# Kernel tuning notes

Measured on AMD Instinct MI355X. Metric: run time of the kernel, lower is better.

Reference implementation:

```python
import jax, jax.numpy as jnp
import numpy as np

HEADS = 8
DIM_HEAD = 128
LN_EPS = 1e-5


def setup_inputs() -> dict:
    key = jax.random.key(0)
    ks = jax.random.split(key, 4)
    N, M, C, V, T = 64, 2, 64, 15, 256
    dim = C * V              # 960
    inner = HEADS * DIM_HEAD # 1024
    return {
        "x": jax.random.normal(ks[0], (N, M, C, V, T), dtype=jnp.float32),
        "ln_g": jnp.ones((dim,), jnp.float32),
        "ln_b": jnp.zeros((dim,), jnp.float32),
        "w_qkv": jax.random.normal(ks[1], (dim, 3 * inner), dtype=jnp.float32) * (dim ** -0.5),
        "w_out": jax.random.normal(ks[2], (inner, dim), dtype=jnp.float32) * (inner ** -0.5),
        "b_out": jnp.zeros((dim,), jnp.float32),
        "w_lin": jax.random.normal(ks[3], (T, T), dtype=jnp.float32) * (T ** -0.5),
        "b_lin": jnp.zeros((T,), jnp.float32),
    }


def reference(x, ln_g, ln_b, w_qkv, w_out, b_out, w_lin, b_lin):
    N, M, C, V, T = x.shape
    dim = C * V
    # [N, M, C, V, T] -> [N*M, T, C*V]
    xs = jnp.transpose(x, (0, 1, 4, 2, 3)).reshape(N * M, T, dim)

    # PreNorm (LayerNorm over last dim)
    mu = jnp.mean(xs, axis=-1, keepdims=True)
    var = jnp.mean(jnp.square(xs - mu), axis=-1, keepdims=True)
    xn = (xs - mu) * jax.lax.rsqrt(var + LN_EPS) * ln_g + ln_b

    # Attention
    qkv = xn @ w_qkv  # [NM, T, 3*inner]
    q, k, v = jnp.split(qkv, 3, axis=-1)
    def to_heads(t):
        return jnp.transpose(t.reshape(N * M, T, HEADS, DIM_HEAD), (0, 2, 1, 3))
    q, k, v = to_heads(q), to_heads(k), to_heads(v)  # [NM, H, T, D]
    scale = DIM_HEAD ** -0.5
    dots = jnp.einsum('nhid,nhjd->nhij', q, k) * scale
    attn = jax.nn.softmax(dots, axis=-1)
    out = jnp.einsum('nhij,nhjd->nhid', attn, v)
    out = jnp.transpose(out, (0, 2, 1, 3)).reshape(N * M, T, HEADS * DIM_HEAD)
    out = out @ w_out + b_out

    # Residual
    xs = out + xs

    # back to [N, M, C, V, T], then Linear over T + tanh
    x2 = jnp.transpose(xs.reshape(N, M, T, C, V), (0, 1, 3, 4, 2))
    y = jnp.tanh(x2 @ w_lin.T + b_lin)
    return y
```

## Files before the change

kernel.cpp:

```cpp
#include <hip/hip_runtime.h>

typedef unsigned short ushort;
using short8 = __attribute__((ext_vector_type(8))) short;
using f32x4  = __attribute__((ext_vector_type(4))) float;
using i32x4  = __attribute__((ext_vector_type(4))) int;
using us4    = __attribute__((ext_vector_type(4))) ushort;

static __device__ __forceinline__ float bf2f(ushort u) {
  union { unsigned int i; float f; } x; x.i = ((unsigned int)u) << 16; return x.f;
}
static __device__ __forceinline__ ushort f2bf(float f) {
  union { float f; unsigned int i; } x; x.f = f;
  unsigned int u = x.i;
  unsigned int r = u + 0x7fffu + ((u >> 16) & 1u);
  return (ushort)(r >> 16);
}

#define GLOAD16(gp, lp)                                                   \
  __builtin_amdgcn_global_load_lds(                                      \
      (const __attribute__((address_space(1))) void*)(gp),               \
      (__attribute__((address_space(3))) void*)(lp), 16, 0, 0)

__global__ __launch_bounds__(256) void wtrans_kernel(const float* __restrict__ in,
                                                     ushort* __restrict__ out,
                                                     int R, int C) {
  __shared__ float sl[32][33];
  int tx = threadIdx.x & 31, ty = threadIdx.x >> 5;
  int c0 = blockIdx.x * 32, r0 = blockIdx.y * 32;
#pragma unroll
  for (int s = 0; s < 4; s++) {
    int r = r0 + ty + s * 8;
    int c = c0 + tx;
    sl[ty + s * 8][tx] = (c < C) ? in[(size_t)r * C + c] : 0.f;
  }
  __syncthreads();
#pragma unroll
  for (int s = 0; s < 4; s++) {
    int c = c0 + ty + s * 8;
    int r = r0 + tx;
    out[(size_t)c * R + r] = f2bf(sl[tx][ty + s * 8]);
  }
}

__global__ void wsplit_kernel(const float* __restrict__ in, ushort* __restrict__ hi,
                              ushort* __restrict__ lo, int n) {
  int i = blockIdx.x * 256 + threadIdx.x;
  if (i < n) {
    float v = in[i];
    ushort h = f2bf(v);
    hi[i] = h;
    lo[i] = f2bf(v - bf2f(h));
  }
}

__global__ __launch_bounds__(256) void ln_part_kernel(const float* __restrict__ x,
                                                      float* __restrict__ part) {
  int nm = blockIdx.y, ch = blockIdx.x, t = threadIdx.x;
  float s = 0.f, ss = 0.f;
  const float* base = x + ((size_t)nm * 960 + (size_t)ch * 240) * 256 + t;
#pragma unroll 4
  for (int r = 0; r < 240; r++) {
    float v = base[(size_t)r * 256];
    s += v; ss += v * v;
  }
  float2 o; o.x = s; o.y = ss;
  ((float2*)part)[(nm * 4 + ch) * 256 + t] = o;
}

__global__ __launch_bounds__(256) void ln_stat_kernel(const float* __restrict__ part,
                                                      float* __restrict__ stat) {
  int nm = blockIdx.x, t = threadIdx.x;
  float s = 0.f, ss = 0.f;
#pragma unroll
  for (int ch = 0; ch < 4; ch++) {
    float2 p = ((const float2*)part)[(nm * 4 + ch) * 256 + t];
    s += p.x; ss += p.y;
  }
  float mean = s * (1.f / 960.f);
  float var = ss * (1.f / 960.f) - mean * mean;
  float2 o; o.x = mean; o.y = rsqrtf(var + 1e-5f);
  ((float2*)stat)[nm * 256 + t] = o;
}

__global__ __launch_bounds__(256) void ln_apply_kernel(const float* __restrict__ x,
                                                       const float* __restrict__ stat,
                                                       const float* __restrict__ g,
                                                       const float* __restrict__ b,
                                                       ushort* __restrict__ xn) {
  __shared__ float sl[64][65];
  int nm = blockIdx.y;
  int tb = blockIdx.x & 3, cvb = blockIdx.x >> 2;
  int t0 = tb * 64, cv0 = cvb * 64;
  int tx = threadIdx.x & 63, ty = threadIdx.x >> 6;
#pragma unroll
  for (int s = 0; s < 16; s++) {
    int r = ty + s * 4;
    sl[r][tx] = x[((size_t)nm * 960 + cv0 + r) * 256 + t0 + tx];
  }
  __syncthreads();
  float gg = g[cv0 + tx], bb = b[cv0 + tx];
#pragma unroll
  for (int s = 0; s < 16; s++) {
    int tt = ty + s * 4;
    float2 ms = ((const float2*)stat)[nm * 256 + t0 + tt];
    float v = (sl[tx][tt] - ms.x) * ms.y * gg + bb;
    xn[((size_t)nm * 256 + t0 + tt) * 960 + cv0 + tx] = f2bf(v);
  }
}

template <int MODE>
__global__ __launch_bounds__(512, 2) void gemm256(
    const ushort* __restrict__ A, int lda, const ushort* __restrict__ BT, int ldb, int nkt,
    const ushort* __restrict__ Alo, const ushort* __restrict__ Blo,
    ushort* __restrict__ o0, ushort* __restrict__ o1, ushort* __restrict__ o2,
    const float* __restrict__ bias, float* __restrict__ fout) {
  __shared__ char smem[131072];
  int tid = threadIdx.x;
  int l = tid & 63, w = tid >> 6;
  int wr = w >> 2, wc = w & 3;
  int lr = l & 15, lg = l >> 4;
  int cb = blockIdx.x * 256, rb = blockIdx.y * 256;

  int srow = tid >> 2;
  int scol = ((tid & 3) ^ ((tid >> 2) & 3)) * 8;

  int swz = (lg ^ (lr & 3)) << 4;
  const char* ArdB = smem + (wr * 128 + lr) * 64 + swz;
  const char* BrdB = smem + 65536 + (wc * 64 + lr) * 64 + swz;

  auto stage_half = [&](int kt, int kk, int isB) {
    const ushort* P; int ld; int k0;
    if (MODE == 2) {
      int seg = kt >> 2; k0 = (kt & 3) * 64 + kk * 32;
      P = isB ? ((seg == 1) ? Blo : BT) : ((seg == 2) ? Alo : A);
      ld = 256;
    } else {
      P = isB ? BT : A; ld = isB ? ldb : lda; k0 = kt * 64 + kk * 32;
    }
    const ushort* gp = P + (size_t)((isB ? cb : rb) + srow) * ld + k0 + scol;
    char* dst = smem + isB * 65536 + (kt & 1) * 32768 + kk * 16384 + tid * 16;
    GLOAD16(gp, dst);
    GLOAD16(gp + (size_t)128 * ld, dst + 8192);
  };

  f32x4 acc[8][4];
#pragma unroll
  for (int i = 0; i < 8; i++)
#pragma unroll
    for (int j = 0; j < 4; j++) acc[i][j] = (f32x4){0.f, 0.f, 0.f, 0.f};

  stage_half(0, 0, 0); stage_half(0, 0, 1); stage_half(0, 1, 0); stage_half(0, 1, 1);
  asm volatile("s_waitcnt vmcnt(4)" ::: "memory");
  __builtin_amdgcn_s_barrier();

  for (int t = 0; t < nkt; t++) {
    const char* Ard = ArdB + (t & 1) * 32768;
    const char* Brd = BrdB + (t & 1) * 32768;
    bool st = (t + 1 < nkt);
    short8 a[4], b[4];

#pragma unroll
    for (int j = 0; j < 4; j++) b[j] = *(const short8*)(Brd + j * 1024);
#pragma unroll
    for (int i = 0; i < 4; i++) a[i] = *(const short8*)(Ard + i * 1024);
    if (st) stage_half(t + 1, 0, 0);
    __builtin_amdgcn_s_barrier();
    __builtin_amdgcn_s_setprio(1);
#pragma unroll
    for (int i = 0; i < 4; i++)
#pragma unroll
      for (int j = 0; j < 4; j++)
        acc[i][j] = __builtin_amdgcn_mfma_f32_16x16x32_bf16(a[i], b[j], acc[i][j], 0, 0, 0);
    __builtin_amdgcn_s_setprio(0);
    __builtin_amdgcn_s_barrier();

#pragma unroll
    for (int i = 0; i < 4; i++) a[i] = *(const short8*)(Ard + (4 + i) * 1024);
    if (st) stage_half(t + 1, 0, 1);
    __builtin_amdgcn_s_barrier();
    __builtin_amdgcn_s_setprio(1);
#pragma unroll
    for (int i = 0; i < 4; i++)
#pragma unroll
      for (int j = 0; j < 4; j++)
        acc[4 + i][j] = __builtin_amdgcn_mfma_f32_16x16x32_bf16(a[i], b[j], acc[4 + i][j], 0, 0, 0);
    __builtin_amdgcn_s_setprio(0);
    if (st) asm volatile("s_waitcnt vmcnt(4)" ::: "memory");
    else    asm volatile("s_waitcnt vmcnt(0)" ::: "memory");
    __builtin_amdgcn_s_barrier();

#pragma unroll
    for (int j = 0; j < 4; j++) b[j] = *(const short8*)(Brd + 16384 + j * 1024);
#pragma unroll
    for (int i = 0; i < 4; i++) a[i] = *(const short8*)(Ard + 16384 + i * 1024);
    if (st) stage_half(t + 1, 1, 0);
    __builtin_amdgcn_s_barrier();
    __builtin_amdgcn_s_setprio(1);
#pragma unroll
    for (int i = 0; i < 4; i++)
#pragma unroll
      for (int j = 0; j < 4; j++)
        acc[i][j] = __builtin_amdgcn_mfma_f32_16x16x32_bf16(a[i], b[j], acc[i][j], 0, 0, 0);
    __builtin_amdgcn_s_setprio(0);
    __builtin_amdgcn_s_barrier();

#pragma unroll
    for (int i = 0; i < 4; i++) a[i] = *(const short8*)(Ard + 16384 + (4 + i) * 1024);
    if (st) stage_half(t + 1, 1, 1);
    __builtin_amdgcn_s_barrier();
    __builtin_amdgcn_s_setprio(1);
#pragma unroll
    for (int i = 0; i < 4; i++)
#pragma unroll
      for (int j = 0; j < 4; j++)
        acc[4 + i][j] = __builtin_amdgcn_mfma_f32_16x16x32_bf16(a[i], b[j], acc[4 + i][j], 0, 0, 0);
    __builtin_amdgcn_s_setprio(0);
    if (st) asm volatile("s_waitcnt vmcnt(4)" ::: "memory");
    else    asm volatile("s_waitcnt vmcnt(0)" ::: "memory");
    __builtin_amdgcn_s_barrier();
  }

  int row0 = rb + wr * 128, col0 = cb + wc * 64;
  if (MODE == 0) {
    int nm = rb >> 8;
    int which = cb >> 10;
#pragma unroll
    for (int i = 0; i < 8; i++)
#pragma unroll
      for (int j = 0; j < 4; j++) {
        f32x4 v = acc[i][j];
        int col = col0 + j * 16 + lr;
        int cl = col & 1023;
        int h = cl >> 7, d = cl & 127;
        int nmh = nm * 8 + h;
        int t0 = wr * 128 + i * 16 + lg * 4;
        if (which == 2) {
          us4 pk;
          pk.x = f2bf(v[0]); pk.y = f2bf(v[1]); pk.z = f2bf(v[2]); pk.w = f2bf(v[3]);
          *(us4*)&o2[((size_t)nmh * 128 + d) * 256 + t0] = pk;
        } else if (which == 0) {
#pragma unroll
          for (int r = 0; r < 4; r++)
            o0[((size_t)nmh * 256 + t0 + r) * 128 + d] = f2bf(v[r] * 0.08838834764831845f);
        } else {
#pragma unroll
          for (int r = 0; r < 4; r++)
            o1[((size_t)nmh * 256 + t0 + r) * 128 + d] = f2bf(v[r]);
        }
      }
  } else if (MODE == 1) {
#pragma unroll
    for (int i = 0; i < 8; i++)
#pragma unroll
      for (int j = 0; j < 4; j++) {
        f32x4 v = acc[i][j];
        int col = col0 + j * 16 + lr;
        float bb = (col < 960) ? bias[col] : 0.f;
#pragma unroll
        for (int r = 0; r < 4; r++) {
          int row = row0 + i * 16 + lg * 4 + r;
          o0[(size_t)row * 1024 + col] = f2bf(v[r] + bb);
        }
      }
  } else {
#pragma unroll
    for (int i = 0; i < 8; i++)
#pragma unroll
      for (int j = 0; j < 4; j++) {
        f32x4 v = acc[i][j];
        int col = col0 + j * 16 + lr;
        float bb = bias[col];
#pragma unroll
        for (int r = 0; r < 4; r++) {
          int row = row0 + i * 16 + lg * 4 + r;
          fout[(size_t)row * 256 + col] = tanhf(v[r] + bb);
        }
      }
  }
}

__global__ __launch_bounds__(256) void attn_kernel(const ushort* __restrict__ q,
                                                   const ushort* __restrict__ kb,
                                                   const ushort* __restrict__ vT,
                                                   ushort* __restrict__ ao) {
  __shared__ ushort KVs[128 * 72];
  __shared__ ushort Ps[64 * 264];
  int tid = threadIdx.x;
  int l = tid & 63, w = tid >> 6;
  int lr = l & 15, lg = l >> 4;
  int qb = blockIdx.x;
  int nmh = blockIdx.y;

  short8 aq[4];
  {
    const ushort* qp = q + ((size_t)nmh * 256 + qb * 64 + w * 16 + lr) * 128 + lg * 8;
#pragma unroll
    for (int kk = 0; kk < 4; kk++) aq[kk] = *(const short8*)(qp + kk * 32);
  }

  f32x4 s_acc[16];
#pragma unroll
  for (int f = 0; f < 16; f++) s_acc[f] = (f32x4){0.f, 0.f, 0.f, 0.f};

  for (int ct = 0; ct < 4; ct++) {
    __syncthreads();
#pragma unroll
    for (int u = 0; u < 4; u++) {
      int i = tid + u * 256;
      int r = i >> 4, c = i & 15;
      *(i32x4*)&KVs[r * 136 + c * 8] =
          *(const i32x4*)(kb + ((size_t)nmh * 256 + ct * 64 + r) * 128 + c * 8);
    }
    __syncthreads();
#pragma unroll
    for (int j = 0; j < 4; j++) {
      short8 bk[4];
#pragma unroll
      for (int kk = 0; kk < 4; kk++)
        bk[kk] = *(const short8*)&KVs[(j * 16 + lr) * 136 + kk * 32 + lg * 8];
#pragma unroll
      for (int kk = 0; kk < 4; kk++)
        s_acc[ct * 4 + j] =
            __builtin_amdgcn_mfma_f32_16x16x32_bf16(aq[kk], bk[kk], s_acc[ct * 4 + j], 0, 0, 0);
    }
  }

  float m[4] = {-1e30f, -1e30f, -1e30f, -1e30f};
#pragma unroll
  for (int f = 0; f < 16; f++)
#pragma unroll
    for (int r = 0; r < 4; r++) m[r] = fmaxf(m[r], s_acc[f][r]);
#pragma unroll
  for (int dd = 1; dd < 16; dd <<= 1)
#pragma unroll
    for (int r = 0; r < 4; r++) m[r] = fmaxf(m[r], __shfl_xor(m[r], dd, 64));
  float sum[4] = {0.f, 0.f, 0.f, 0.f};
#pragma unroll
  for (int f = 0; f < 16; f++)
#pragma unroll
    for (int r = 0; r < 4; r++) {
      float p = __expf(s_acc[f][r] - m[r]);
      s_acc[f][r] = p;
      sum[r] += p;
    }
#pragma unroll
  for (int dd = 1; dd < 16; dd <<= 1)
#pragma unroll
    for (int r = 0; r < 4; r++) sum[r] += __shfl_xor(sum[r], dd, 64);
  float rs[4];
#pragma unroll
  for (int r = 0; r < 4; r++) rs[r] = 1.f / sum[r];

#pragma unroll
  for (int f = 0; f < 16; f++)
#pragma unroll
    for (int r = 0; r < 4; r++)
      Ps[(w * 16 + lg * 4 + r) * 264 + f * 16 + lr] = f2bf(s_acc[f][r]);

  f32x4 o_acc[8];
#pragma unroll
  for (int j = 0; j < 8; j++) o_acc[j] = (f32x4){0.f, 0.f, 0.f, 0.f};

  for (int ct = 0; ct < 4; ct++) {
    __syncthreads();
#pragma unroll
    for (int u = 0; u < 4; u++) {
      int i = tid + u * 256;
      int r = i >> 3, c = i & 7;
      *(i32x4*)&KVs[r * 72 + c * 8] =
          *(const i32x4*)(vT + ((size_t)nmh * 128 + r) * 256 + ct * 64 + c * 8);
    }
    __syncthreads();
#pragma unroll
    for (int kk = 0; kk < 2; kk++) {
      short8 ap = *(const short8*)&Ps[(w * 16 + lr) * 264 + ct * 64 + kk * 32 + lg * 8];
#pragma unroll
      for (int j = 0; j < 8; j++) {
        short8 bv = *(const short8*)&KVs[(j * 16 + lr) * 72 + kk * 32 + lg * 8];
        o_acc[j] = __builtin_amdgcn_mfma_f32_16x16x32_bf16(ap, bv, o_acc[j], 0, 0, 0);
      }
    }
  }

  int nm = nmh >> 3, h = nmh & 7;
  int trow0 = qb * 64 + w * 16;
#pragma unroll
  for (int j = 0; j < 8; j++)
#pragma unroll
    for (int r = 0; r < 4; r++) {
      int t = trow0 + lg * 4 + r;
      int d = h * 128 + j * 16 + lr;
      ao[((size_t)nm * 256 + t) * 1024 + d] = f2bf(o_acc[j][r] * rs[r]);
    }
}

__global__ __launch_bounds__(256) void x2split_kernel(const float* __restrict__ x,
                                                      const ushort* __restrict__ proj,
                                                      ushort* __restrict__ hi,
                                                      ushort* __restrict__ lo) {
  __shared__ ushort sl[64][65];
  int nm = blockIdx.y;
  int tb = blockIdx.x & 3, cvb = blockIdx.x >> 2;
  int t0 = tb * 64, cv0 = cvb * 64;
  int tx = threadIdx.x & 63, ty = threadIdx.x >> 6;
#pragma unroll
  for (int s = 0; s < 16; s++) {
    int r = ty + s * 4;
    sl[r][tx] = proj[((size_t)nm * 256 + t0 + r) * 1024 + cv0 + tx];
  }
  __syncthreads();
#pragma unroll
  for (int s = 0; s < 16; s++) {
    int cvl = ty + s * 4;
    size_t R = (size_t)nm * 960 + cv0 + cvl;
    float v = x[R * 256 + t0 + tx] + bf2f(sl[tx][cvl]);
    ushort h = f2bf(v);
    hi[R * 256 + t0 + tx] = h;
    lo[R * 256 + t0 + tx] = f2bf(v - bf2f(h));
  }
}

extern "C" void kernel_launch(void* const* d_in, const int* in_sizes, int n_in,
                              void* d_out, int out_size, void* d_ws, size_t ws_size,
                              hipStream_t stream) {
  const float* x = (const float*)d_in[0];
  const float* ln_g = (const float*)d_in[1];
  const float* ln_b = (const float*)d_in[2];
  const float* w_qkv = (const float*)d_in[3];
  const float* w_out = (const float*)d_in[4];
  const float* b_out = (const float*)d_in[5];
  const float* w_lin = (const float*)d_in[6];
  const float* b_lin = (const float*)d_in[7];
  float* out = (float*)d_out;

  char* ws = (char*)d_ws;
  size_t off = 0;
  auto alloc = [&](size_t bytes) -> void* {
    void* p = ws + off;
    off = (off + bytes + 255) & ~(size_t)255;
    return p;
  };

  ushort* wqkvT = (ushort*)alloc((size_t)3072 * 960 * 2);
  ushort* woutT = (ushort*)alloc((size_t)1024 * 1024 * 2);
  ushort* whi   = (ushort*)alloc((size_t)65536 * 2);
  ushort* wlo   = (ushort*)alloc((size_t)65536 * 2);
  float*  part  = (float*)alloc((size_t)128 * 4 * 256 * 2 * 4);
  float*  stat  = (float*)alloc((size_t)32768 * 2 * 4);
  ushort* xn    = (ushort*)alloc((size_t)32768 * 960 * 2);
  ushort* qbuf  = (ushort*)alloc((size_t)1024 * 256 * 128 * 2);
  ushort* kbuf  = (ushort*)alloc((size_t)1024 * 256 * 128 * 2);
  ushort* vTbuf = (ushort*)alloc((size_t)1024 * 256 * 128 * 2);
  ushort* attnout = (ushort*)alloc((size_t)32768 * 1024 * 2);
  ushort* proj = qbuf;
  ushort* x2hi = kbuf;
  ushort* x2lo = vTbuf;

  wtrans_kernel<<<dim3(96, 30), 256, 0, stream>>>(w_qkv, wqkvT, 960, 3072);
  wtrans_kernel<<<dim3(32, 32), 256, 0, stream>>>(w_out, woutT, 1024, 960);
  wsplit_kernel<<<dim3(256), 256, 0, stream>>>(w_lin, whi, wlo, 65536);

  ln_part_kernel<<<dim3(4, 128), 256, 0, stream>>>(x, part);
  ln_stat_kernel<<<dim3(128), 256, 0, stream>>>(part, stat);
  ln_apply_kernel<<<dim3(60, 128), 256, 0, stream>>>(x, stat, ln_g, ln_b, xn);

  gemm256<0><<<dim3(12, 128), 512, 0, stream>>>(xn, 960, wqkvT, 960, 15, nullptr, nullptr,
                                                qbuf, kbuf, vTbuf, nullptr, nullptr);
  attn_kernel<<<dim3(4, 1024), 256, 0, stream>>>(qbuf, kbuf, vTbuf, attnout);
  gemm256<1><<<dim3(4, 128), 512, 0, stream>>>(attnout, 1024, woutT, 1024, 16, nullptr, nullptr,
                                               proj, nullptr, nullptr, b_out, nullptr);
  x2split_kernel<<<dim3(60, 128), 256, 0, stream>>>(x, proj, x2hi, x2lo);
  gemm256<2><<<dim3(1, 480), 512, 0, stream>>>(x2hi, 256, whi, 256, 12, x2lo, wlo,
                                               nullptr, nullptr, nullptr, b_lin, out);
}
```

Measured before the change: 691.4 us.

## Fuse LayerNorm into one kernel and change GEMM LDS swizzle

Replaces the three LayerNorm kernels (partial sums, stats, apply) with a single kernel. Each block stages a 960x16 column slab of x in LDS, reduces the mean and rstd with shuffles, and writes normalized bf16 directly. This reads x once instead of twice and drops two launches and the intermediate buffers. It also changes the XOR swizzle pattern for LDS staging and reads in the GEMM to reduce bank conflicts. The fused kernel uses about 77KB of LDS, which limits occupancy, and its 64-byte strided loads from x may coalesce less well.

```diff
diff --git a/kernel.cpp b/kernel.cpp
--- a/kernel.cpp
+++ b/kernel.cpp
@@ -53,58 +53,61 @@
   }
 }
 
-__global__ __launch_bounds__(256) void ln_part_kernel(const float* __restrict__ x,
-                                                      float* __restrict__ part) {
-  int nm = blockIdx.y, ch = blockIdx.x, t = threadIdx.x;
-  float s = 0.f, ss = 0.f;
-  const float* base = x + ((size_t)nm * 960 + (size_t)ch * 240) * 256 + t;
-#pragma unroll 4
-  for (int r = 0; r < 240; r++) {
-    float v = base[(size_t)r * 256];
-    s += v; ss += v * v;
-  }
-  float2 o; o.x = s; o.y = ss;
-  ((float2*)part)[(nm * 4 + ch) * 256 + t] = o;
-}
-
-__global__ __launch_bounds__(256) void ln_stat_kernel(const float* __restrict__ part,
-                                                      float* __restrict__ stat) {
-  int nm = blockIdx.x, t = threadIdx.x;
-  float s = 0.f, ss = 0.f;
-#pragma unroll
-  for (int ch = 0; ch < 4; ch++) {
-    float2 p = ((const float2*)part)[(nm * 4 + ch) * 256 + t];
-    s += p.x; ss += p.y;
-  }
-  float mean = s * (1.f / 960.f);
-  float var = ss * (1.f / 960.f) - mean * mean;
-  float2 o; o.x = mean; o.y = rsqrtf(var + 1e-5f);
-  ((float2*)stat)[nm * 256 + t] = o;
-}
-
-__global__ __launch_bounds__(256) void ln_apply_kernel(const float* __restrict__ x,
-                                                       const float* __restrict__ stat,
+__global__ __launch_bounds__(256) void ln_fused_kernel(const float* __restrict__ x,
                                                        const float* __restrict__ g,
                                                        const float* __restrict__ b,
                                                        ushort* __restrict__ xn) {
-  __shared__ float sl[64][65];
+  __shared__ float sl[960][20];
+  __shared__ float smean[16], srstd[16];
+  int tid = threadIdx.x;
   int nm = blockIdx.y;
-  int tb = blockIdx.x & 3, cvb = blockIdx.x >> 2;
-  int t0 = tb * 64, cv0 = cvb * 64;
-  int tx = threadIdx.x & 63, ty = threadIdx.x >> 6;
-#pragma unroll
-  for (int s = 0; s < 16; s++) {
-    int r = ty + s * 4;
-    sl[r][tx] = x[((size_t)nm * 960 + cv0 + r) * 256 + t0 + tx];
+  int t0 = blockIdx.x * 16;
+
+  int r0 = tid >> 2, c4 = (tid & 3) * 4;
+#pragma unroll
+  for (int it = 0; it < 15; it++) {
+    int r = it * 64 + r0;
+    float4 v = *(const float4*)&x[((size_t)nm * 960 + r) * 256 + t0 + c4];
+    *(float4*)&sl[r][c4] = v;
   }
   __syncthreads();
-  float gg = g[cv0 + tx], bb = b[cv0 + tx];
-#pragma unroll
-  for (int s = 0; s < 16; s++) {
-    int tt = ty + s * 4;
-    float2 ms = ((const float2*)stat)[nm * 256 + t0 + tt];
-    float v = (sl[tx][tt] - ms.x) * ms.y * gg + bb;
-    xn[((size_t)nm * 256 + t0 + tt) * 960 + cv0 + tx] = f2bf(v);
+
+  int tg = tid >> 4, lt = tid & 15;
+  float s = 0.f, ss = 0.f;
+#pragma unroll 4
+  for (int k = 0; k < 60; k++) {
+    float v = sl[lt + k * 16][tg];
+    s += v; ss += v * v;
+  }
+#pragma unroll
+  for (int d = 1; d < 16; d <<= 1) {
+    s += __shfl_xor(s, d, 64);
+    ss += __shfl_xor(ss, d, 64);
+  }
+  if (lt == 0) {
+    float mean = s * (1.f / 960.f);
+    float var = ss * (1.f / 960.f) - mean * mean;
+    smean[tg] = mean;
+    srstd[tg] = rsqrtf(var + 1e-5f);
+  }
+  __syncthreads();
+
+  float gg[4], bb[4];
+#pragma unroll
+  for (int c = 0; c < 4; c++) {
+    int col = c * 256 + tid;
+    if (col < 960) { gg[c] = g[col]; bb[c] = b[col]; }
+  }
+#pragma unroll
+  for (int t = 0; t < 16; t++) {
+    float mean = smean[t], rstd = srstd[t];
+#pragma unroll
+    for (int c = 0; c < 4; c++) {
+      int col = c * 256 + tid;
+      if (col < 960)
+        xn[((size_t)nm * 256 + t0 + t) * 960 + col] =
+            f2bf((sl[col][t] - mean) * rstd * gg[c] + bb[c]);
+    }
   }
 }
 
@@ -122,9 +125,9 @@
   int cb = blockIdx.x * 256, rb = blockIdx.y * 256;
 
   int srow = tid >> 2;
-  int scol = ((tid & 3) ^ ((tid >> 2) & 3)) * 8;
-
-  int swz = (lg ^ (lr & 3)) << 4;
+  int scol = ((tid & 3) ^ ((tid >> 3) & 3)) * 8;
+
+  int swz = (lg ^ ((lr >> 1) & 3)) << 4;
   const char* ArdB = smem + (wr * 128 + lr) * 64 + swz;
   const char* BrdB = smem + 65536 + (wc * 64 + lr) * 64 + swz;
 
@@ -445,8 +448,6 @@
   ushort* woutT = (ushort*)alloc((size_t)1024 * 1024 * 2);
   ushort* whi   = (ushort*)alloc((size_t)65536 * 2);
   ushort* wlo   = (ushort*)alloc((size_t)65536 * 2);
-  float*  part  = (float*)alloc((size_t)128 * 4 * 256 * 2 * 4);
-  float*  stat  = (float*)alloc((size_t)32768 * 2 * 4);
   ushort* xn    = (ushort*)alloc((size_t)32768 * 960 * 2);
   ushort* qbuf  = (ushort*)alloc((size_t)1024 * 256 * 128 * 2);
   ushort* kbuf  = (ushort*)alloc((size_t)1024 * 256 * 128 * 2);
@@ -460,9 +461,7 @@
   wtrans_kernel<<<dim3(32, 32), 256, 0, stream>>>(w_out, woutT, 1024, 960);
   wsplit_kernel<<<dim3(256), 256, 0, stream>>>(w_lin, whi, wlo, 65536);
 
-  ln_part_kernel<<<dim3(4, 128), 256, 0, stream>>>(x, part);
-  ln_stat_kernel<<<dim3(128), 256, 0, stream>>>(part, stat);
-  ln_apply_kernel<<<dim3(60, 128), 256, 0, stream>>>(x, stat, ln_g, ln_b, xn);
+  ln_fused_kernel<<<dim3(16, 128), 256, 0, stream>>>(x, ln_g, ln_b, xn);
 
   gemm256<0><<<dim3(12, 128), 512, 0, stream>>>(xn, 960, wqkvT, 960, 15, nullptr, nullptr,
                                                 qbuf, kbuf, vTbuf, nullptr, nullptr);
```

After: 683.7 us. Within noise of the previous version (-1.1%).
